# Optimization experiments

Measured on AMD Instinct MI355X. Metric: run time of the kernel, lower is better.

## Reference

```python
import jax, jax.numpy as jnp
import numpy as np

DX = 0.1
DY = 0.1
W_B = 1000.0
W_PARALLEL = 1000.0
W_DIV = 100.0
EPS = 1e-10


def setup_inputs() -> dict:
    key = jax.random.key(0)
    k1, k2 = jax.random.split(key)
    outputs = jax.random.normal(k1, (2, 3, 256, 256, 64), dtype=jnp.float32)
    targets = jax.random.normal(k2, (2, 4, 256, 256, 64), dtype=jnp.float32)
    return {"outputs": outputs, "targets": targets}


def _corners(f):
    # 8 shifted views f[..., i:, j:, k:] (with 0 -> [0:-1], 1 -> [1:]) on dims 2,3,4
    s0, s1 = slice(0, -1), slice(1, None)
    return {(i, j, k): f[:, :, (s1 if i else s0), (s1 if j else s0), (s1 if k else s0)]
            for i in (0, 1) for j in (0, 1) for k in (0, 1)}


def _forward(outputs, targets):
    bx_p, by_p, bz_p = outputs[:, 0:1], outputs[:, 1:2], outputs[:, 2:3]
    bx_t, by_t, bz_t = targets[:, 0:1], targets[:, 1:2], targets[:, 2:3]

    loss_b = (jnp.mean((bx_p**2 + by_p**2 - bx_t**2 - by_t**2) ** 2 / (bx_t**2 + by_t**2 + EPS))
              + jnp.mean((bz_p - bz_t) ** 4 / (bz_t**2 + EPS)))
    loss_parallel = jnp.mean((bx_p * by_t - by_p * bx_t) ** 2
                             / (bx_t**2 + by_t**2 + bz_t**2 + EPS))

    bx = _corners(bx_p)
    by = _corners(by_p)
    bz = _corners(bz_p)
    z = _corners(targets[:, 3:4])

    num = (0.25 * (bx[1, 0, 0] + bx[1, 1, 0] + bx[1, 0, 1] + bx[1, 1, 1]) * DY * 0.5 * (z[1, 0, 1] - z[1, 0, 0] + z[1, 1, 1] - z[1, 1, 0])
           - 0.25 * (bx[0, 0, 0] + bx[0, 1, 0] + bx[0, 0, 1] + bx[0, 1, 1]) * DY * 0.5 * (z[0, 0, 1] - z[0, 0, 0] + z[0, 1, 1] - z[0, 1, 0])
           + 0.25 * (by[0, 1, 0] + by[1, 1, 0] + by[0, 1, 1] + by[1, 1, 1]) * DX * 0.5 * (z[0, 1, 1] - z[0, 1, 0] + z[1, 1, 1] - z[1, 1, 0])
           - 0.25 * (by[0, 0, 0] + by[1, 0, 0] + by[0, 0, 1] + by[1, 0, 1]) * DX * 0.5 * (z[0, 0, 1] - z[0, 0, 0] + z[1, 0, 1] - z[1, 0, 0])
           + 0.25 * (bz[0, 0, 1] + bz[0, 1, 1] + bz[1, 0, 1] + bz[1, 1, 1]) * DX * DY
           - 0.25 * (bz[0, 0, 0] + bz[0, 1, 0] + bz[1, 0, 0] + bz[1, 1, 0]) * DX * DY
           + (bx[0, 0, 1] + bx[1, 0, 1] + bx[1, 1, 1]) * DY * (z[0, 0, 1] - z[1, 0, 1]) / 6
           + (bx[0, 1, 1] + bx[1, 1, 1] + bx[1, 0, 1]) * DY * (z[0, 1, 1] - z[1, 1, 1]) / 6
           + (by[1, 0, 1] + by[1, 1, 1] + by[0, 1, 1]) * DX * (z[1, 0, 1] - z[1, 1, 1]) / 6
           + (by[0, 0, 1] + by[0, 1, 1] + by[1, 1, 1]) * DX * (z[0, 0, 1] - z[0, 1, 1]) / 6
           - (bx[0, 0, 0] + bx[1, 0, 0] + bx[1, 1, 0]) * DY * (z[0, 0, 0] - z[1, 0, 0]) / 6
           - (bx[0, 1, 0] + bx[1, 1, 0] + bx[1, 0, 0]) * DY * (z[0, 1, 0] - z[1, 1, 0]) / 6
           - (by[1, 0, 0] + by[1, 1, 0] + by[0, 1, 0]) * DX * (z[1, 0, 0] - z[1, 1, 0]) / 6
           - (by[0, 0, 0] + by[0, 1, 0] + by[1, 1, 0]) * DX * (z[0, 0, 0] - z[0, 1, 0]) / 6)

    bx_c = sum(bx[c] for c in sorted(bx)) * 0.125
    by_c = sum(by[c] for c in sorted(by)) * 0.125
    bz_c = sum(bz[c] for c in sorted(bz)) * 0.125
    den = bx_c**2 + by_c**2 + bz_c**2 + EPS

    loss_div = jnp.mean(num**2 / den) / DX**2 / DY**2

    return (W_B * loss_b + W_PARALLEL * loss_parallel, W_DIV * loss_div)


def reference(outputs, targets):
    return _forward(outputs, targets)
```

## Files before the change

### kernel.cpp

```cpp
#include <hip/hip_runtime.h>
#include <stdint.h>

constexpr int B = 2, X = 256, Y = 256, Z = 64;
constexpr int CO = X * Y * Z;
constexpr int YZ = Y * Z;
constexpr long long N_PTS   = (long long)B * X * Y * Z;
constexpr long long M_CELLS = (long long)B * (X-1) * (Y-1) * (Z-1);

constexpr int RPB = 16;
constexpr int XS  = 16;
constexpr int TPB = 256;
constexpr int WPB = TPB / 64;
constexpr int BLOCKS = B * (Y / RPB) * (X / XS);

constexpr int CHS  = 1152;
constexpr int BUFS = 4 * CHS;

#define EPSc 1e-10f
#define SIXTH (1.0f / 6.0f)
#define RCPF(v) __builtin_amdgcn_rcpf(v)

typedef float fvec4 __attribute__((ext_vector_type(4)));

#define F4C(v, c) (((c) == 0) ? (v).x : ((c) == 1) ? (v).y : ((c) == 2) ? (v).z : (v).w)

typedef const __attribute__((address_space(1))) uint32_t* gptr_t;
typedef __attribute__((address_space(3))) uint32_t* lptr_t;

__global__ __launch_bounds__(TPB, 2) void loss_main(const float* __restrict__ outs,
                                                    const float* __restrict__ tgts,
                                                    double* __restrict__ partial) {
    __shared__ __align__(16) float sm[3 * BUFS];

    const int lane = threadIdx.x & 63;
    const int wv   = threadIdx.x >> 6;
    const int blk  = blockIdx.x;

    const int b  = blk >> 8;
    const int r  = blk & 255;
    const int sy = r >> 4;
    const int xc = r & 15;
    const int y0 = sy * RPB;
    const int x0 = xc * XS;

    const float* ob = outs + (size_t)b * 3 * CO;
    const float* tb = tgts + (size_t)b * 4 * CO;

    const int row_l = wv * 4 + (lane >> 4);
    const int zi    = (lane & 15) << 2;
    const int y_own = y0 + row_l;
    const bool yvalid = (y_own < Y - 1);
    const int y16 = (y0 + 16 < Y) ? (y0 + 16) : (Y - 1);

    const float* chbase = (wv < 3) ? (ob + (size_t)wv * CO) : (tb + (size_t)3 * CO);

    const float* tnt = tb + (size_t)y_own * Z + zi;

    auto stage = [&](int xs, float* buf) {
        const float* gbase = chbase + (size_t)xs * YZ;
        float* ldst = buf + wv * CHS;
        const float* gsrc = gbase + (size_t)y0 * Z;
        #pragma unroll
        for (int k = 0; k < 4; ++k) {
            __builtin_amdgcn_global_load_lds((gptr_t)(gsrc + k * 256 + lane * 4),
                                             (lptr_t)(ldst + k * 256 + lane * 4),
                                             16, 0, 0);
        }
        __builtin_amdgcn_global_load_lds((gptr_t)(gbase + (size_t)y16 * Z + lane),
                                         (lptr_t)(ldst + 16 * 64 + lane),
                                         4, 0, 0);
    };

    float* prv = sm + 2 * BUFS;
    float* cur = sm;
    float* nxt = sm + BUFS;

    stage(x0, cur);
    fvec4 tc0, tc1, tc2;
    fvec4 tn0 = {0,0,0,0}, tn1 = {0,0,0,0}, tn2 = {0,0,0,0};
    {
        const float* p = tnt + (size_t)x0 * YZ;
        tc0 = __builtin_nontemporal_load((const fvec4*)(p + 0 * CO));
        tc1 = __builtin_nontemporal_load((const fvec4*)(p + 1 * CO));
        tc2 = __builtin_nontemporal_load((const fvec4*)(p + 2 * CO));
    }
    __syncthreads();

    double s_pt = 0.0, s_dv = 0.0;

    #define SMF4(base, ch, row) (*(const fvec4*)((base) + (ch) * CHS + (row) * 64 + zi))

    #pragma unroll 1
    for (int i = 0; i <= XS; ++i) {
        if (i < XS) {
            int xs1 = x0 + i + 1;
            if (xs1 > X - 1) xs1 = X - 1;
            stage(xs1, nxt);
            if (i + 1 < XS) {
                const float* p = tnt + (size_t)(x0 + i + 1) * YZ;
                tn0 = __builtin_nontemporal_load((const fvec4*)(p + 0 * CO));
                tn1 = __builtin_nontemporal_load((const fvec4*)(p + 1 * CO));
                tn2 = __builtin_nontemporal_load((const fvec4*)(p + 2 * CO));
            }
        }

        if (i < XS) {
            const fvec4 obx = SMF4(cur, 0, row_l);
            const fvec4 oby = SMF4(cur, 1, row_l);
            const fvec4 obz = SMF4(cur, 2, row_l);
            float pt4 = 0.0f;
            #pragma unroll
            for (int c = 0; c < 4; ++c) {
                const float bxp = F4C(obx, c), byp = F4C(oby, c), bzp = F4C(obz, c);
                const float bxt = F4C(tc0, c), byt = F4C(tc1, c), bzt = F4C(tc2, c);
                const float bxt2 = bxt * bxt, byt2 = byt * byt, bzt2 = bzt * bzt;
                const float dxy = bxt2 + byt2;
                const float t1 = bxp * bxp + byp * byp - dxy;
                const float e1 = t1 * t1 * RCPF(dxy + EPSc);
                const float dd = bzp - bzt;
                const float dd2 = dd * dd;
                const float e2 = dd2 * dd2 * RCPF(bzt2 + EPSc);
                const float cr = bxp * byt - byp * bxt;
                const float e3 = cr * cr * RCPF(dxy + bzt2 + EPSc);
                pt4 += e1 + e2 + e3;
            }
            s_pt += (double)pt4;
        }

        if (i >= 1 && (x0 + i - 1) < X - 1) {
            const fvec4 obx   = SMF4(prv, 0, row_l);
            const fvec4 oby   = SMF4(prv, 1, row_l);
            const fvec4 obz   = SMF4(prv, 2, row_l);
            const fvec4 tzc   = SMF4(prv, 3, row_l);
            const fvec4 obx1  = SMF4(cur, 0, row_l);
            const fvec4 oby1  = SMF4(cur, 1, row_l);
            const fvec4 obz1  = SMF4(cur, 2, row_l);
            const fvec4 tzc1  = SMF4(cur, 3, row_l);
            const fvec4 obxy  = SMF4(prv, 0, row_l + 1);
            const fvec4 obyy  = SMF4(prv, 1, row_l + 1);
            const fvec4 obzy  = SMF4(prv, 2, row_l + 1);
            const fvec4 tzcy  = SMF4(prv, 3, row_l + 1);
            const fvec4 obxy1 = SMF4(cur, 0, row_l + 1);
            const fvec4 obyy1 = SMF4(cur, 1, row_l + 1);
            const fvec4 obzy1 = SMF4(cur, 2, row_l + 1);
            const fvec4 tzcy1 = SMF4(cur, 3, row_l + 1);

            float sxp[5], sxm[5], syp[5], sym[5];
            float zxp[5], zxm[5], zyp[5], zym[5];
            float Sx[5], Sy[5], Sz[5], G2[5];

            #pragma unroll
            for (int t = 0; t < 4; ++t) {
                const float bx00 = F4C(obx, t),   bx10 = F4C(obx1, t);
                const float bx01 = F4C(obxy, t),  bx11 = F4C(obxy1, t);
                const float by00 = F4C(oby, t),   by10 = F4C(oby1, t);
                const float by01 = F4C(obyy, t),  by11 = F4C(obyy1, t);
                const float bz00 = F4C(obz, t),   bz10 = F4C(obz1, t);
                const float bz01 = F4C(obzy, t),  bz11 = F4C(obzy1, t);
                const float zc00 = F4C(tzc, t),   zc10 = F4C(tzc1, t);
                const float zc01 = F4C(tzcy, t),  zc11 = F4C(tzcy1, t);

                sxp[t] = bx10 + bx11;   sxm[t] = bx00 + bx01;
                syp[t] = by01 + by11;   sym[t] = by00 + by10;
                zxp[t] = zc10 + zc11;   zxm[t] = zc00 + zc01;
                zyp[t] = zc01 + zc11;   zym[t] = zc00 + zc10;
                Sx[t] = sxp[t] + sxm[t];
                Sy[t] = syp[t] + sym[t];
                Sz[t] = (bz00 + bz01) + (bz10 + bz11);
                G2[t] = 0.025f * Sz[t]
                      + SIXTH * ((bx00 + sxp[t]) * (zc00 - zc10)
                               + (bx01 + sxp[t]) * (zc01 - zc11)
                               + (by10 + syp[t]) * (zc10 - zc11)
                               + (by00 + syp[t]) * (zc00 - zc01));
            }
            sxp[4] = __shfl_down(sxp[0], 1);
            sxm[4] = __shfl_down(sxm[0], 1);
            syp[4] = __shfl_down(syp[0], 1);
            sym[4] = __shfl_down(sym[0], 1);
            zxp[4] = __shfl_down(zxp[0], 1);
            zxm[4] = __shfl_down(zxm[0], 1);
            zyp[4] = __shfl_down(zyp[0], 1);
            zym[4] = __shfl_down(zym[0], 1);
            Sz[4]  = __shfl_down(Sz[0],  1);
            G2[4]  = __shfl_down(G2[0],  1);
            Sx[4] = sxp[4] + sxm[4];
            Sy[4] = syp[4] + sym[4];

            float dv4 = 0.0f;
            #pragma unroll
            for (int c = 0; c < 4; ++c) {
                const float fx = (sxp[c] + sxp[c+1]) * (zxp[c+1] - zxp[c])
                               - (sxm[c] + sxm[c+1]) * (zxm[c+1] - zxm[c])
                               + (syp[c] + syp[c+1]) * (zyp[c+1] - zyp[c])
                               - (sym[c] + sym[c+1]) * (zym[c+1] - zym[c]);
                const float num2 = 0.125f * fx + (G2[c+1] - G2[c]);
                const float SxS = Sx[c] + Sx[c+1];
                const float SyS = Sy[c] + Sy[c+1];
                const float SzS = Sz[c] + Sz[c+1];
                const float q = SxS * SxS + SyS * SyS + SzS * SzS;
                const float den = 0.015625f * q + EPSc;
                const float v = num2 * num2 * RCPF(den);
                const bool ok = yvalid && ((zi + c) < Z - 1);
                dv4 += ok ? v : 0.0f;
            }
            s_dv += (double)dv4;
        }

        if (i < XS) __syncthreads();

        float* tmp = prv; prv = cur; cur = nxt; nxt = tmp;
        tc0 = tn0; tc1 = tn1; tc2 = tn2;
    }

    for (int off = 32; off > 0; off >>= 1) {
        s_pt += __shfl_down(s_pt, off);
        s_dv += __shfl_down(s_dv, off);
    }

    __shared__ double lds_pt[WPB];
    __shared__ double lds_dv[WPB];
    if (lane == 0) { lds_pt[wv] = s_pt; lds_dv[wv] = s_dv; }
    __syncthreads();
    if (threadIdx.x == 0) {
        double p = 0.0, d = 0.0;
        #pragma unroll
        for (int w = 0; w < WPB; ++w) { p += lds_pt[w]; d += lds_dv[w]; }
        partial[2 * blockIdx.x]     = p;
        partial[2 * blockIdx.x + 1] = d;
    }
}

__global__ __launch_bounds__(256) void loss_finalize(const double* __restrict__ partial,
                                                     float* __restrict__ out) {
    double s0 = 0.0, s1 = 0.0;
    for (int i = threadIdx.x; i < BLOCKS; i += 256) {
        s0 += partial[2 * i];
        s1 += partial[2 * i + 1];
    }
    const int lane = threadIdx.x & 63;
    const int wave = threadIdx.x >> 6;
    for (int off = 32; off > 0; off >>= 1) {
        s0 += __shfl_down(s0, off);
        s1 += __shfl_down(s1, off);
    }
    __shared__ double l0[4], l1[4];
    if (lane == 0) { l0[wave] = s0; l1[wave] = s1; }
    __syncthreads();
    if (threadIdx.x == 0) {
        double p = 0.0, d = 0.0;
        #pragma unroll
        for (int w = 0; w < 4; ++w) { p += l0[w]; d += l1[w]; }
        const double out0 = 1000.0 * (p / (double)N_PTS);
        const double out1 = 10000.0 * (d / (double)M_CELLS);
        out[0] = (float)out0;
        out[1] = (float)out1;
    }
}

extern "C" void kernel_launch(void* const* d_in, const int* in_sizes, int n_in,
                              void* d_out, int out_size, void* d_ws, size_t ws_size,
                              hipStream_t stream) {
    const float* outs = (const float*)d_in[0];
    const float* tgts = (const float*)d_in[1];
    float* out = (float*)d_out;
    double* partial = (double*)d_ws;

    loss_main<<<BLOCKS, TPB, 0, stream>>>(outs, tgts, partial);
    loss_finalize<<<1, 256, 0, stream>>>(partial, out);
}
```

Before: 247.6 us.

## Carry previous x-plane in registers, double-buffer LDS, raise occupancy, swizzle blocks

The previous x-slice is now kept in registers instead of a third LDS buffer, so LDS drops from triple to double buffering and the per-channel stride is trimmed. Launch bounds are raised to allow four blocks per CU. Target loads are issued in the same iteration rather than prefetched one step ahead, and block indices are remapped across groups of eight so neighbouring blocks spread out, presumably across XCDs. This costs extra register pressure from holding eight vec4s across iterations and removes the prefetch of target data.

New measurement: 266.8 us. 1.08x slower.

```diff
diff --git a/kernel.cpp b/kernel.cpp
--- a/kernel.cpp
+++ b/kernel.cpp
@@ -13,7 +13,7 @@
 constexpr int WPB = TPB / 64;
 constexpr int BLOCKS = B * (Y / RPB) * (X / XS);
 
-constexpr int CHS  = 1152;
+constexpr int CHS  = 1088;
 constexpr int BUFS = 4 * CHS;
 
 #define EPSc 1e-10f
@@ -27,14 +27,15 @@
 typedef const __attribute__((address_space(1))) uint32_t* gptr_t;
 typedef __attribute__((address_space(3))) uint32_t* lptr_t;
 
-__global__ __launch_bounds__(TPB, 2) void loss_main(const float* __restrict__ outs,
+__global__ __launch_bounds__(TPB, 4) void loss_main(const float* __restrict__ outs,
                                                     const float* __restrict__ tgts,
                                                     double* __restrict__ partial) {
-    __shared__ __align__(16) float sm[3 * BUFS];
+    __shared__ __align__(16) float sm[2 * BUFS];
 
     const int lane = threadIdx.x & 63;
     const int wv   = threadIdx.x >> 6;
-    const int blk  = blockIdx.x;
+
+    const int blk = ((int)blockIdx.x & 7) * (BLOCKS / 8) + ((int)blockIdx.x >> 3);
 
     const int b  = blk >> 8;
     const int r  = blk & 255;
@@ -71,94 +72,59 @@
                                          4, 0, 0);
     };
 
-    float* prv = sm + 2 * BUFS;
     float* cur = sm;
     float* nxt = sm + BUFS;
 
     stage(x0, cur);
-    fvec4 tc0, tc1, tc2;
-    fvec4 tn0 = {0,0,0,0}, tn1 = {0,0,0,0}, tn2 = {0,0,0,0};
-    {
-        const float* p = tnt + (size_t)x0 * YZ;
-        tc0 = __builtin_nontemporal_load((const fvec4*)(p + 0 * CO));
-        tc1 = __builtin_nontemporal_load((const fvec4*)(p + 1 * CO));
-        tc2 = __builtin_nontemporal_load((const fvec4*)(p + 2 * CO));
-    }
     __syncthreads();
 
     double s_pt = 0.0, s_dv = 0.0;
+
+    fvec4 p0r0 = {0,0,0,0}, p1r0 = {0,0,0,0}, p2r0 = {0,0,0,0}, p3r0 = {0,0,0,0};
+    fvec4 p0r1 = {0,0,0,0}, p1r1 = {0,0,0,0}, p2r1 = {0,0,0,0}, p3r1 = {0,0,0,0};
 
     #define SMF4(base, ch, row) (*(const fvec4*)((base) + (ch) * CHS + (row) * 64 + zi))
 
     #pragma unroll 1
     for (int i = 0; i <= XS; ++i) {
+        const fvec4 c0r0 = SMF4(cur, 0, row_l);
+        const fvec4 c1r0 = SMF4(cur, 1, row_l);
+        const fvec4 c2r0 = SMF4(cur, 2, row_l);
+        const fvec4 c3r0 = SMF4(cur, 3, row_l);
+        const fvec4 c0r1 = SMF4(cur, 0, row_l + 1);
+        const fvec4 c1r1 = SMF4(cur, 1, row_l + 1);
+        const fvec4 c2r1 = SMF4(cur, 2, row_l + 1);
+        const fvec4 c3r1 = SMF4(cur, 3, row_l + 1);
+
+        fvec4 tc0 = {0,0,0,0}, tc1 = {0,0,0,0}, tc2 = {0,0,0,0};
+        if (i < XS) {
+            const float* p = tnt + (size_t)(x0 + i) * YZ;
+            tc0 = __builtin_nontemporal_load((const fvec4*)(p + 0 * CO));
+            tc1 = __builtin_nontemporal_load((const fvec4*)(p + 1 * CO));
+            tc2 = __builtin_nontemporal_load((const fvec4*)(p + 2 * CO));
+        }
+
         if (i < XS) {
             int xs1 = x0 + i + 1;
             if (xs1 > X - 1) xs1 = X - 1;
             stage(xs1, nxt);
-            if (i + 1 < XS) {
-                const float* p = tnt + (size_t)(x0 + i + 1) * YZ;
-                tn0 = __builtin_nontemporal_load((const fvec4*)(p + 0 * CO));
-                tn1 = __builtin_nontemporal_load((const fvec4*)(p + 1 * CO));
-                tn2 = __builtin_nontemporal_load((const fvec4*)(p + 2 * CO));
-            }
-        }
-
-        if (i < XS) {
-            const fvec4 obx = SMF4(cur, 0, row_l);
-            const fvec4 oby = SMF4(cur, 1, row_l);
-            const fvec4 obz = SMF4(cur, 2, row_l);
-            float pt4 = 0.0f;
-            #pragma unroll
-            for (int c = 0; c < 4; ++c) {
-                const float bxp = F4C(obx, c), byp = F4C(oby, c), bzp = F4C(obz, c);
-                const float bxt = F4C(tc0, c), byt = F4C(tc1, c), bzt = F4C(tc2, c);
-                const float bxt2 = bxt * bxt, byt2 = byt * byt, bzt2 = bzt * bzt;
-                const float dxy = bxt2 + byt2;
-                const float t1 = bxp * bxp + byp * byp - dxy;
-                const float e1 = t1 * t1 * RCPF(dxy + EPSc);
-                const float dd = bzp - bzt;
-                const float dd2 = dd * dd;
-                const float e2 = dd2 * dd2 * RCPF(bzt2 + EPSc);
-                const float cr = bxp * byt - byp * bxt;
-                const float e3 = cr * cr * RCPF(dxy + bzt2 + EPSc);
-                pt4 += e1 + e2 + e3;
-            }
-            s_pt += (double)pt4;
         }
 
         if (i >= 1 && (x0 + i - 1) < X - 1) {
-            const fvec4 obx   = SMF4(prv, 0, row_l);
-            const fvec4 oby   = SMF4(prv, 1, row_l);
-            const fvec4 obz   = SMF4(prv, 2, row_l);
-            const fvec4 tzc   = SMF4(prv, 3, row_l);
-            const fvec4 obx1  = SMF4(cur, 0, row_l);
-            const fvec4 oby1  = SMF4(cur, 1, row_l);
-            const fvec4 obz1  = SMF4(cur, 2, row_l);
-            const fvec4 tzc1  = SMF4(cur, 3, row_l);
-            const fvec4 obxy  = SMF4(prv, 0, row_l + 1);
-            const fvec4 obyy  = SMF4(prv, 1, row_l + 1);
-            const fvec4 obzy  = SMF4(prv, 2, row_l + 1);
-            const fvec4 tzcy  = SMF4(prv, 3, row_l + 1);
-            const fvec4 obxy1 = SMF4(cur, 0, row_l + 1);
-            const fvec4 obyy1 = SMF4(cur, 1, row_l + 1);
-            const fvec4 obzy1 = SMF4(cur, 2, row_l + 1);
-            const fvec4 tzcy1 = SMF4(cur, 3, row_l + 1);
-
             float sxp[5], sxm[5], syp[5], sym[5];
             float zxp[5], zxm[5], zyp[5], zym[5];
             float Sx[5], Sy[5], Sz[5], G2[5];
 
             #pragma unroll
             for (int t = 0; t < 4; ++t) {
-                const float bx00 = F4C(obx, t),   bx10 = F4C(obx1, t);
-                const float bx01 = F4C(obxy, t),  bx11 = F4C(obxy1, t);
-                const float by00 = F4C(oby, t),   by10 = F4C(oby1, t);
-                const float by01 = F4C(obyy, t),  by11 = F4C(obyy1, t);
-                const float bz00 = F4C(obz, t),   bz10 = F4C(obz1, t);
-                const float bz01 = F4C(obzy, t),  bz11 = F4C(obzy1, t);
-                const float zc00 = F4C(tzc, t),   zc10 = F4C(tzc1, t);
-                const float zc01 = F4C(tzcy, t),  zc11 = F4C(tzcy1, t);
+                const float bx00 = F4C(p0r0, t),  bx10 = F4C(c0r0, t);
+                const float bx01 = F4C(p0r1, t),  bx11 = F4C(c0r1, t);
+                const float by00 = F4C(p1r0, t),  by10 = F4C(c1r0, t);
+                const float by01 = F4C(p1r1, t),  by11 = F4C(c1r1, t);
+                const float bz00 = F4C(p2r0, t),  bz10 = F4C(c2r0, t);
+                const float bz01 = F4C(p2r1, t),  bz11 = F4C(c2r1, t);
+                const float zc00 = F4C(p3r0, t),  zc10 = F4C(c3r0, t);
+                const float zc01 = F4C(p3r1, t),  zc11 = F4C(c3r1, t);
 
                 sxp[t] = bx10 + bx11;   sxm[t] = bx00 + bx01;
                 syp[t] = by01 + by11;   sym[t] = by00 + by10;
@@ -206,10 +172,31 @@
             s_dv += (double)dv4;
         }
 
+        if (i < XS) {
+            float pt4 = 0.0f;
+            #pragma unroll
+            for (int c = 0; c < 4; ++c) {
+                const float bxp = F4C(c0r0, c), byp = F4C(c1r0, c), bzp = F4C(c2r0, c);
+                const float bxt = F4C(tc0, c), byt = F4C(tc1, c), bzt = F4C(tc2, c);
+                const float bxt2 = bxt * bxt, byt2 = byt * byt, bzt2 = bzt * bzt;
+                const float dxy = bxt2 + byt2;
+                const float t1 = bxp * bxp + byp * byp - dxy;
+                const float e1 = t1 * t1 * RCPF(dxy + EPSc);
+                const float dd = bzp - bzt;
+                const float dd2 = dd * dd;
+                const float e2 = dd2 * dd2 * RCPF(bzt2 + EPSc);
+                const float cr = bxp * byt - byp * bxt;
+                const float e3 = cr * cr * RCPF(dxy + bzt2 + EPSc);
+                pt4 += e1 + e2 + e3;
+            }
+            s_pt += (double)pt4;
+        }
+
         if (i < XS) __syncthreads();
 
-        float* tmp = prv; prv = cur; cur = nxt; nxt = tmp;
-        tc0 = tn0; tc1 = tn1; tc2 = tn2;
+        p0r0 = c0r0; p1r0 = c1r0; p2r0 = c2r0; p3r0 = c3r0;
+        p0r1 = c0r1; p1r1 = c1r1; p2r1 = c2r1; p3r1 = c3r1;
+        float* tmp = cur; cur = nxt; nxt = tmp;
     }
 
     for (int off = 32; off > 0; off >>= 1) {
@@ -225,8 +212,8 @@
         double p = 0.0, d = 0.0;
         #pragma unroll
         for (int w = 0; w < WPB; ++w) { p += lds_pt[w]; d += lds_dv[w]; }
-        partial[2 * blockIdx.x]     = p;
-        partial[2 * blockIdx.x + 1] = d;
+        partial[2 * blk]     = p;
+        partial[2 * blk + 1] = d;
     }
 }
 
```
